# Optimization experiments

Measured on AMD Instinct MI355X. Metric: run time of the kernel, lower is better.

The kernel has to match this reference:

```python
import jax, jax.numpy as jnp
import numpy as np

B, C_LEN, Q_LEN, H = 16, 2048, 128, 128
NEG = -1000000000.0


def setup_inputs() -> dict:
    key = jax.random.key(0)
    k1, k2, k3, k4, k5 = jax.random.split(key, 5)
    context = jax.random.normal(k1, (B, C_LEN, H), dtype=jnp.float32)
    query = jax.random.normal(k2, (B, Q_LEN, H), dtype=jnp.float32)
    W = jax.random.normal(k3, (3 * H,), dtype=jnp.float32) * (1.0 / np.sqrt(3 * H))
    context_mask = jax.random.randint(k4, (B, C_LEN), 0, 2).astype(jnp.int32)
    query_mask = jax.random.randint(k5, (B, Q_LEN), 0, 2).astype(jnp.int32)
    return {"context": context, "query": query, "W": W,
            "context_mask": context_mask, "query_mask": query_mask}


def reference(context, query, W, context_mask, query_mask):
    h = context.shape[-1]
    # Decompose W([c; q; c*q]) into three rank-1 terms -> avoid (B,c,q,3h) tensor.
    w_c, w_q, w_cq = W[:h], W[h:2 * h], W[2 * h:]
    s_c = context @ w_c                                   # (B, c_len)
    s_q = query @ w_q                                     # (B, q_len)
    s_cq = jnp.einsum('bch,bqh->bcq', context * w_cq, query)
    S = s_c[:, :, None] + s_q[:, None, :] + s_cq          # (B, c_len, q_len)
    # query mask -> C2Q attention
    S = jnp.where(query_mask[:, None, :] == 0, NEG, S)
    a = jax.nn.softmax(S, axis=-1)
    c2q = jnp.einsum('bcq,bqh->bch', a, query)
    # context mask -> Q2C attention over max-over-query scores
    S_for_q2c = jnp.where(context_mask[:, :, None] == 0, NEG, S)
    max_q = jnp.max(S_for_q2c, axis=-1)                   # (B, c_len)
    max_q = jnp.where(context_mask == 0, NEG, max_q)
    b = jax.nn.softmax(max_q, axis=-1)
    q2c = jnp.einsum('bc,bch->bh', b, context)            # (B, h)
    G = jnp.concatenate(
        [context, c2q, context * c2q, context * q2c[:, None, :]], axis=-1)
    return G  # (B, c_len, 4h)
```

## Files before the change

kernel.cpp:

```cpp
#include <hip/hip_runtime.h>
#include <math.h>

#define B_ 16
#define C_ 2048
#define Q_ 128
#define H_ 128
#define NEGV (-1000000000.0f)
#define REC_ 136

typedef short short8 __attribute__((ext_vector_type(8)));
typedef float f32x16 __attribute__((ext_vector_type(16)));
typedef float f32x4 __attribute__((ext_vector_type(4)));

__device__ __forceinline__ short f2bf(float f) {
  unsigned u = __builtin_bit_cast(unsigned, f);
  u += 0x7fffu + ((u >> 16) & 1u);
  return (short)(u >> 16);
}

__device__ __forceinline__ int swz(int row, int ch) {
  return row * 128 + (((ch ^ (row & 7)) & 15) << 3);
}

__device__ __forceinline__ void nt_store4(float* p, float4 v) {
  __builtin_nontemporal_store(__builtin_bit_cast(f32x4, v), (f32x4*)p);
}

__device__ __forceinline__ float wave_max(float v) {
#pragma unroll
  for (int off = 32; off; off >>= 1) v = fmaxf(v, __shfl_xor(v, off, 64));
  return v;
}
__device__ __forceinline__ float wave_sum(float v) {
#pragma unroll
  for (int off = 32; off; off >>= 1) v += __shfl_xor(v, off, 64);
  return v;
}

__global__ __launch_bounds__(512, 4) void k1_main(
    const float* __restrict__ ctx, const float* __restrict__ qry,
    const float* __restrict__ W, const int* __restrict__ cmask,
    const int* __restrict__ qmask, float* __restrict__ out,
    float* __restrict__ pw) {
  __shared__ short QXs[16384];
  __shared__ short Xs[64 * 128];
  __shared__ float scv[64];
  __shared__ float sqm[128];
  __shared__ float pm_lds[4][64];
  __shared__ float ps_lds[4][64];
  __shared__ float mcv[64];
  __shared__ float wcv[64];
  __shared__ float mzl[2];
  __shared__ float pqacc[4][128];

  int b = blockIdx.x >> 5;
  int ct = blockIdx.x & 31;
  int tid = threadIdx.x;
  int bc0 = b * C_ + ct * 64;

  {
    int c = tid >> 3, part = tid & 7;
    const float* crow = ctx + (size_t)(bc0 + c) * H_;
    float* orow = out + (size_t)(bc0 + c) * (4 * H_);
    float wsum = 0.f;
#pragma unroll
    for (int jj = 0; jj < 4; jj++) {
      int k = part + 8 * jj;
      float4 v = *(const float4*)&crow[4 * k];
      nt_store4(&orow[4 * k], v);
      float4 wc = *(const float4*)&W[4 * k];
      float4 wq = *(const float4*)&W[2 * H_ + 4 * k];
      wsum += v.x * wc.x + v.y * wc.y + v.z * wc.z + v.w * wc.w;
      short4 xp;
      xp.x = f2bf(v.x * wq.x);
      xp.y = f2bf(v.y * wq.y);
      xp.z = f2bf(v.z * wq.z);
      xp.w = f2bf(v.w * wq.w);
      *(short4*)&Xs[swz(c, k >> 1) + (k & 1) * 4] = xp;
    }
    wsum += __shfl_xor(wsum, 1, 64);
    wsum += __shfl_xor(wsum, 2, 64);
    wsum += __shfl_xor(wsum, 4, 64);
    if (part == 0) scv[c] = wsum;
  }
  {
    int q = tid >> 2, p = tid & 3;
    const float* qrow = qry + (size_t)(b * Q_ + q) * H_;
    float s = 0.f;
#pragma unroll
    for (int jj = 0; jj < 8; jj++) {
      int k = p + 4 * jj;
      float4 v = *(const float4*)&qrow[4 * k];
      float4 wq4 = *(const float4*)&W[H_ + 4 * k];
      s += v.x * wq4.x + v.y * wq4.y + v.z * wq4.z + v.w * wq4.w;
      short4 pk;
      pk.x = f2bf(v.x); pk.y = f2bf(v.y); pk.z = f2bf(v.z); pk.w = f2bf(v.w);
      *(short4*)&QXs[swz(q, k >> 1) + (k & 1) * 4] = pk;
    }
    s += __shfl_xor(s, 1, 64);
    s += __shfl_xor(s, 2, 64);
    if (p == 0) sqm[q] = qmask[b * Q_ + q] ? s : -1e12f;
  }
  __syncthreads();

  int w = tid >> 6, lane = tid & 63;
  int lq = lane & 31, kg = lane >> 5;

  int wm = w >> 1, wn = w & 1;
  f32x16 acc;
#pragma unroll
  for (int r = 0; r < 16; r++) acc[r] = 0.f;
  {
    int rA = wm * 32 + lq, rB = wn * 32 + lq;
#pragma unroll
    for (int ks = 0; ks < 8; ks++) {
      int ch = 2 * ks + kg;
      short8 a = *(const short8*)&QXs[swz(rA, ch)];
      short8 bb = *(const short8*)&Xs[swz(rB, ch)];
      acc = __builtin_amdgcn_mfma_f32_32x32x16_bf16(a, bb, acc, 0, 0, 0);
    }
  }

  int cL = wn * 32 + lq;
  float scc = scv[cL];
  float pmax = -3e38f;
#pragma unroll
  for (int g = 0; g < 4; g++) {
    int q0 = wm * 32 + 8 * g + 4 * kg;
    float4 s4 = *(const float4*)&sqm[q0];
    float sv[4] = {s4.x, s4.y, s4.z, s4.w};
#pragma unroll
    for (int r = 0; r < 4; r++) {
      float Sv = acc[4 * g + r] + scc + sv[r];
      acc[4 * g + r] = Sv;
      pmax = fmaxf(pmax, Sv);
    }
  }
  pmax = fmaxf(pmax, __shfl_xor(pmax, 32, 64));
  if (lane < 32) pm_lds[wm][cL] = pmax;
  __syncthreads();

  float M = fmaxf(fmaxf(pm_lds[0][cL], pm_lds[1][cL]),
                  fmaxf(pm_lds[2][cL], pm_lds[3][cL]));
  if (wm == 0 && lane < 32) {
    mcv[cL] = cmask[bc0 + cL] ? M : NEGV;
  }
  float psum = 0.f;
#pragma unroll
  for (int g = 0; g < 4; g++) {
    int q0 = wm * 32 + 8 * g + 4 * kg;
    float e0 = __expf(acc[4 * g + 0] - M);
    float e1 = __expf(acc[4 * g + 1] - M);
    float e2 = __expf(acc[4 * g + 2] - M);
    float e3 = __expf(acc[4 * g + 3] - M);
    psum += e0 + e1 + e2 + e3;
    short4 pk;
    pk.x = f2bf(e0); pk.y = f2bf(e1); pk.z = f2bf(e2); pk.w = f2bf(e3);
    *(short4*)&Xs[swz(cL, q0 >> 3) + (q0 & 7)] = pk;
  }
  psum += __shfl_xor(psum, 32, 64);
  if (lane < 32) ps_lds[wm][cL] = psum;

  {
    int qp = tid >> 3, p = tid & 7;
    const float* q0r = qry + (size_t)(b * Q_ + 2 * qp) * H_;
    const float* q1r = q0r + H_;
#pragma unroll
    for (int jj = 0; jj < 4; jj++) {
      int k = p + 8 * jj;
      float4 v0 = *(const float4*)&q0r[4 * k];
      float4 v1 = *(const float4*)&q1r[4 * k];
      const float* f0 = (const float*)&v0;
      const float* f1 = (const float*)&v1;
#pragma unroll
      for (int e = 0; e < 4; e++) {
        int h = 4 * k + e;
        short2 pr;
        pr.x = f2bf(f0[e]);
        pr.y = f2bf(f1[e]);
        *(short2*)&QXs[swz(h, qp >> 2) + ((2 * qp) & 7)] = pr;
      }
    }
  }
  __syncthreads();

  int wm2 = w & 1, wn2 = w >> 1;
  f32x16 o;
#pragma unroll
  for (int r = 0; r < 16; r++) o[r] = 0.f;
  {
    int rA = wm2 * 32 + lq, rB = wn2 * 32 + lq;
#pragma unroll
    for (int ks = 0; ks < 8; ks++) {
      int ch = 2 * ks + kg;
      short8 af = *(const short8*)&Xs[swz(rA, ch)];
      short8 bf_ = *(const short8*)&QXs[swz(rB, ch)];
      o = __builtin_amdgcn_mfma_f32_32x32x16_bf16(af, bf_, o, 0, 0, 0);
    }
  }

  int h = wn2 * 32 + lq;
#pragma unroll
  for (int g = 0; g < 4; g++) {
    int c0 = wm2 * 32 + 8 * g + 4 * kg;
    float4 z0 = *(const float4*)&ps_lds[0][c0];
    float4 z1 = *(const float4*)&ps_lds[1][c0];
    float4 z2 = *(const float4*)&ps_lds[2][c0];
    float4 z3 = *(const float4*)&ps_lds[3][c0];
    float zz[4] = {z0.x + z1.x + z2.x + z3.x, z0.y + z1.y + z2.y + z3.y,
                   z0.z + z1.z + z2.z + z3.z, z0.w + z1.w + z2.w + z3.w};
#pragma unroll
    for (int r = 0; r < 4; r++) {
      int c = c0 + r;
      float rz = 1.f / zz[r];
      size_t ro = (size_t)(bc0 + c) * (4 * H_);
      float ov = o[4 * g + r] * rz;
      float cv = ctx[(size_t)(bc0 + c) * H_ + h];
      out[ro + H_ + h] = ov;
      out[ro + 2 * H_ + h] = ov * cv;
    }
  }

  if (tid < 64) {
    float mv = mcv[tid];
    float lm = wave_max(mv);
    float ew = __expf(mv - lm);
    wcv[tid] = ew;
    float lz = wave_sum(ew);
    if (tid == 0) { mzl[0] = lm; mzl[1] = lz; }
  }
  __syncthreads();
  {
    int hh = tid & 127, grp = tid >> 7;
    const float* cb = ctx + (size_t)bc0 * H_;
    float a = 0.f;
#pragma unroll
    for (int i = 0; i < 16; i++) {
      int c = grp * 16 + i;
      a += wcv[c] * cb[(size_t)c * H_ + hh];
    }
    pqacc[grp][hh] = a;
  }
  __syncthreads();
  float* rec = pw + (size_t)blockIdx.x * REC_;
  if (tid < 128) {
    rec[8 + tid] = pqacc[0][tid] + pqacc[1][tid] + pqacc[2][tid] + pqacc[3][tid];
  }
  if (tid == 128) rec[0] = mzl[0];
  if (tid == 129) rec[1] = mzl[1];
}

__global__ __launch_bounds__(256) void k4_out(const float* __restrict__ ctx,
                                              const float* __restrict__ pw,
                                              float* __restrict__ out) {
  __shared__ float q2cs[128];
  int b = blockIdx.x >> 5;
  int ct = blockIdx.x & 31;
  int tid = threadIdx.x;
  int bc0 = b * C_ + ct * 64;

  if (tid < 128) {
    const float* base = pw + (size_t)b * 32 * REC_;
    float Mg = -3e38f;
#pragma unroll
    for (int t = 0; t < 32; t++) Mg = fmaxf(Mg, base[t * REC_]);
    float Zg = 0.f, s = 0.f;
#pragma unroll
    for (int t = 0; t < 32; t++) {
      float et = __expf(base[t * REC_] - Mg);
      Zg += et * base[t * REC_ + 1];
      s += et * base[t * REC_ + 8 + tid];
    }
    q2cs[tid] = s / Zg;
  }
  __syncthreads();

  int c = tid >> 2, part = tid & 3;
  const float* crow = ctx + (size_t)(bc0 + c) * H_;
  float* orow = out + (size_t)(bc0 + c) * (4 * H_) + 3 * H_;
#pragma unroll
  for (int jj = 0; jj < 8; jj++) {
    int k = part + 4 * jj;
    float4 v = *(const float4*)&crow[4 * k];
    float4 g = *(const float4*)&q2cs[4 * k];
    nt_store4(&orow[4 * k],
              make_float4(v.x * g.x, v.y * g.y, v.z * g.z, v.w * g.w));
  }
}

extern "C" void kernel_launch(void* const* d_in, const int* in_sizes, int n_in,
                              void* d_out, int out_size, void* d_ws,
                              size_t ws_size, hipStream_t stream) {
  const float* ctx = (const float*)d_in[0];
  const float* qry = (const float*)d_in[1];
  const float* W = (const float*)d_in[2];
  const int* cmask = (const int*)d_in[3];
  const int* qmask = (const int*)d_in[4];
  float* out = (float*)d_out;
  float* pw = (float*)d_ws;

  k1_main<<<B_ * 32, 512, 0, stream>>>(ctx, qry, W, cmask, qmask, out, pw);
  k4_out<<<B_ * 32, 256, 0, stream>>>(ctx, pw, out);
}
```

Baseline: 28.51 us.

## Precompute bf16 query and query scores in a pre-kernel, fuse Q2C accumulation

Adds a small pre-kernel that converts the query to bf16 once and computes masked query scores, so each of the 32 context-tile blocks per batch no longer repeats that conversion and reads half the bytes. The main kernel loads the first GEMM's A operand straight from global bf16, builds the transposed query tile in LDS early, and folds the Q2C weighted context sum into the c2q output loop, reusing the already-loaded context values. c2q stores become nontemporal. This costs an extra kernel launch and adds a barrier placement change.

```diff
diff --git a/kernel.cpp b/kernel.cpp
--- a/kernel.cpp
+++ b/kernel.cpp
@@ -25,6 +25,9 @@
 __device__ __forceinline__ void nt_store4(float* p, float4 v) {
   __builtin_nontemporal_store(__builtin_bit_cast(f32x4, v), (f32x4*)p);
 }
+__device__ __forceinline__ void nt_store1(float* p, float v) {
+  __builtin_nontemporal_store(v, p);
+}
 
 __device__ __forceinline__ float wave_max(float v) {
 #pragma unroll
@@ -37,13 +40,34 @@
   return v;
 }
 
+__global__ __launch_bounds__(256) void k0_pre(const float* __restrict__ qry,
+                                              const float* __restrict__ W,
+                                              const int* __restrict__ qmask,
+                                              short* __restrict__ qb,
+                                              float* __restrict__ sqm_g) {
+  int t = blockIdx.x * 256 + threadIdx.x;
+  int row = t >> 5, l = t & 31;
+  float4 v = *(const float4*)&qry[(size_t)row * H_ + 4 * l];
+  float4 wq = *(const float4*)&W[H_ + 4 * l];
+  float s = v.x * wq.x + v.y * wq.y + v.z * wq.z + v.w * wq.w;
+  short4 pk;
+  pk.x = f2bf(v.x); pk.y = f2bf(v.y); pk.z = f2bf(v.z); pk.w = f2bf(v.w);
+  *(short4*)&qb[(size_t)row * H_ + 4 * l] = pk;
+  s += __shfl_xor(s, 1, 64);
+  s += __shfl_xor(s, 2, 64);
+  s += __shfl_xor(s, 4, 64);
+  s += __shfl_xor(s, 8, 64);
+  s += __shfl_xor(s, 16, 64);
+  if (l == 0) sqm_g[row] = qmask[row] ? s : -1e12f;
+}
+
 __global__ __launch_bounds__(512, 4) void k1_main(
-    const float* __restrict__ ctx, const float* __restrict__ qry,
+    const float* __restrict__ ctx, const short* __restrict__ qb,
     const float* __restrict__ W, const int* __restrict__ cmask,
-    const int* __restrict__ qmask, float* __restrict__ out,
+    const float* __restrict__ sqm_g, float* __restrict__ out,
     float* __restrict__ pw) {
-  __shared__ short QXs[16384];
-  __shared__ short Xs[64 * 128];
+  __shared__ short QTs[16384];
+  __shared__ short Xs[8192];
   __shared__ float scv[64];
   __shared__ float sqm[128];
   __shared__ float pm_lds[4][64];
@@ -51,7 +75,7 @@
   __shared__ float mcv[64];
   __shared__ float wcv[64];
   __shared__ float mzl[2];
-  __shared__ float pqacc[4][128];
+  __shared__ float pq2[2][128];
 
   int b = blockIdx.x >> 5;
   int ct = blockIdx.x & 31;
@@ -84,23 +108,24 @@
     if (part == 0) scv[c] = wsum;
   }
   {
-    int q = tid >> 2, p = tid & 3;
-    const float* qrow = qry + (size_t)(b * Q_ + q) * H_;
-    float s = 0.f;
-#pragma unroll
-    for (int jj = 0; jj < 8; jj++) {
-      int k = p + 4 * jj;
-      float4 v = *(const float4*)&qrow[4 * k];
-      float4 wq4 = *(const float4*)&W[H_ + 4 * k];
-      s += v.x * wq4.x + v.y * wq4.y + v.z * wq4.z + v.w * wq4.w;
-      short4 pk;
-      pk.x = f2bf(v.x); pk.y = f2bf(v.y); pk.z = f2bf(v.z); pk.w = f2bf(v.w);
-      *(short4*)&QXs[swz(q, k >> 1) + (k & 1) * 4] = pk;
-    }
-    s += __shfl_xor(s, 1, 64);
-    s += __shfl_xor(s, 2, 64);
-    if (p == 0) sqm[q] = qmask[b * Q_ + q] ? s : -1e12f;
-  }
+    int qp = tid >> 3, p = tid & 7;
+    const short* r0 = qb + ((size_t)b * Q_ + 2 * qp) * H_;
+    const short* r1 = r0 + H_;
+#pragma unroll
+    for (int pass = 0; pass < 2; pass++) {
+      int h0 = p * 8 + pass * 64;
+      short8 v0 = *(const short8*)&r0[h0];
+      short8 v1 = *(const short8*)&r1[h0];
+#pragma unroll
+      for (int e = 0; e < 8; e++) {
+        short2 pr;
+        pr.x = v0[e];
+        pr.y = v1[e];
+        *(short2*)&QTs[swz(h0 + e, qp >> 2) + ((2 * qp) & 7)] = pr;
+      }
+    }
+  }
+  if (tid < 128) sqm[tid] = sqm_g[b * Q_ + tid];
   __syncthreads();
 
   int w = tid >> 6, lane = tid & 63;
@@ -111,11 +136,12 @@
 #pragma unroll
   for (int r = 0; r < 16; r++) acc[r] = 0.f;
   {
-    int rA = wm * 32 + lq, rB = wn * 32 + lq;
+    const short* arow = qb + ((size_t)b * Q_ + wm * 32 + lq) * H_;
+    int rB = wn * 32 + lq;
 #pragma unroll
     for (int ks = 0; ks < 8; ks++) {
       int ch = 2 * ks + kg;
-      short8 a = *(const short8*)&QXs[swz(rA, ch)];
+      short8 a = *(const short8*)&arow[ch * 8];
       short8 bb = *(const short8*)&Xs[swz(rB, ch)];
       acc = __builtin_amdgcn_mfma_f32_32x32x16_bf16(a, bb, acc, 0, 0, 0);
     }
@@ -160,29 +186,16 @@
   }
   psum += __shfl_xor(psum, 32, 64);
   if (lane < 32) ps_lds[wm][cL] = psum;
-
-  {
-    int qp = tid >> 3, p = tid & 7;
-    const float* q0r = qry + (size_t)(b * Q_ + 2 * qp) * H_;
-    const float* q1r = q0r + H_;
-#pragma unroll
-    for (int jj = 0; jj < 4; jj++) {
-      int k = p + 8 * jj;
-      float4 v0 = *(const float4*)&q0r[4 * k];
-      float4 v1 = *(const float4*)&q1r[4 * k];
-      const float* f0 = (const float*)&v0;
-      const float* f1 = (const float*)&v1;
-#pragma unroll
-      for (int e = 0; e < 4; e++) {
-        int h = 4 * k + e;
-        short2 pr;
-        pr.x = f2bf(f0[e]);
-        pr.y = f2bf(f1[e]);
-        *(short2*)&QXs[swz(h, qp >> 2) + ((2 * qp) & 7)] = pr;
-      }
-    }
-  }
-  __syncthreads();
+  __syncthreads();
+
+  if (tid < 64) {
+    float mv = mcv[tid];
+    float lm = wave_max(mv);
+    float ew = __expf(mv - lm);
+    wcv[tid] = ew;
+    float lz = wave_sum(ew);
+    if (tid == 0) { mzl[0] = lm; mzl[1] = lz; }
+  }
 
   int wm2 = w & 1, wn2 = w >> 1;
   f32x16 o;
@@ -194,12 +207,14 @@
     for (int ks = 0; ks < 8; ks++) {
       int ch = 2 * ks + kg;
       short8 af = *(const short8*)&Xs[swz(rA, ch)];
-      short8 bf_ = *(const short8*)&QXs[swz(rB, ch)];
+      short8 bf_ = *(const short8*)&QTs[swz(rB, ch)];
       o = __builtin_amdgcn_mfma_f32_32x32x16_bf16(af, bf_, o, 0, 0, 0);
     }
   }
+  __syncthreads();
 
   int h = wn2 * 32 + lq;
+  float part = 0.f;
 #pragma unroll
   for (int g = 0; g < 4; g++) {
     int c0 = wm2 * 32 + 8 * g + 4 * kg;
@@ -216,36 +231,17 @@
       size_t ro = (size_t)(bc0 + c) * (4 * H_);
       float ov = o[4 * g + r] * rz;
       float cv = ctx[(size_t)(bc0 + c) * H_ + h];
-      out[ro + H_ + h] = ov;
-      out[ro + 2 * H_ + h] = ov * cv;
-    }
-  }
-
-  if (tid < 64) {
-    float mv = mcv[tid];
-    float lm = wave_max(mv);
-    float ew = __expf(mv - lm);
-    wcv[tid] = ew;
-    float lz = wave_sum(ew);
-    if (tid == 0) { mzl[0] = lm; mzl[1] = lz; }
-  }
-  __syncthreads();
-  {
-    int hh = tid & 127, grp = tid >> 7;
-    const float* cb = ctx + (size_t)bc0 * H_;
-    float a = 0.f;
-#pragma unroll
-    for (int i = 0; i < 16; i++) {
-      int c = grp * 16 + i;
-      a += wcv[c] * cb[(size_t)c * H_ + hh];
-    }
-    pqacc[grp][hh] = a;
-  }
-  __syncthreads();
+      nt_store1(&out[ro + H_ + h], ov);
+      nt_store1(&out[ro + 2 * H_ + h], ov * cv);
+      part += wcv[c] * cv;
+    }
+  }
+  part += __shfl_xor(part, 32, 64);
+  if (kg == 0) pq2[wm2][h] = part;
+  __syncthreads();
+
   float* rec = pw + (size_t)blockIdx.x * REC_;
-  if (tid < 128) {
-    rec[8 + tid] = pqacc[0][tid] + pqacc[1][tid] + pqacc[2][tid] + pqacc[3][tid];
-  }
+  if (tid < 128) rec[8 + tid] = pq2[0][tid] + pq2[1][tid];
   if (tid == 128) rec[0] = mzl[0];
   if (tid == 129) rec[1] = mzl[1];
 }
@@ -297,8 +293,12 @@
   const int* cmask = (const int*)d_in[3];
   const int* qmask = (const int*)d_in[4];
   float* out = (float*)d_out;
-  float* pw = (float*)d_ws;
-
-  k1_main<<<B_ * 32, 512, 0, stream>>>(ctx, qry, W, cmask, qmask, out, pw);
+
+  short* qb = (short*)d_ws;
+  float* sqm_g = (float*)((char*)d_ws + (size_t)B_ * Q_ * H_ * sizeof(short));
+  float* pw = sqm_g + B_ * Q_;
+
+  k0_pre<<<256, 256, 0, stream>>>(qry, W, qmask, qb, sqm_g);
+  k1_main<<<B_ * 32, 512, 0, stream>>>(ctx, qb, W, cmask, sqm_g, out, pw);
   k4_out<<<B_ * 32, 256, 0, stream>>>(ctx, pw, out);
 }
```

Measured after the change: 30.44 us. 1.07x slower.
